# Kernel tuning notes

Measured on AMD Instinct MI355X. Metric: run time of the kernel, lower is better.

Reference implementation:

```python
import jax, jax.numpy as jnp
import numpy as np

N, E = 50000, 800000
IN, MAP, H, O = 256, 64, 4, 64
LEAKY_SLOPE = 0.2


def setup_inputs() -> dict:
    key = jax.random.key(0)
    ks = jax.random.split(key, 12)
    x = jax.random.normal(ks[0], (N, IN), dtype=jnp.float32)
    src = jax.random.randint(ks[1], (E,), 0, N, dtype=jnp.int32)
    dst = jax.random.randint(ks[2], (E,), 0, N, dtype=jnp.int32)
    s = 1.0 / np.sqrt(IN)
    W_gat = jax.random.normal(ks[3], (IN, H * O), dtype=jnp.float32) * s
    attn_l = jax.random.normal(ks[4], (H, O), dtype=jnp.float32) * 0.1
    attn_r = jax.random.normal(ks[5], (H, O), dtype=jnp.float32) * 0.1
    gate_m_W = jax.random.normal(ks[6], (IN, MAP), dtype=jnp.float32) * s
    gate_m_b = jnp.zeros((MAP,), dtype=jnp.float32)
    gate_fn_W = jax.random.normal(ks[7], (2 * IN + MAP, H), dtype=jnp.float32) * (1.0 / np.sqrt(2 * IN + MAP))
    gate_fn_b = jnp.zeros((H,), dtype=jnp.float32)
    merge_W = jax.random.normal(ks[8], (IN + O, O), dtype=jnp.float32) * (1.0 / np.sqrt(IN + O))
    merge_b = jnp.zeros((O,), dtype=jnp.float32)
    return {"x": x, "src": src, "dst": dst, "W_gat": W_gat, "attn_l": attn_l,
            "attn_r": attn_r, "gate_m_W": gate_m_W, "gate_m_b": gate_m_b,
            "gate_fn_W": gate_fn_W, "gate_fn_b": gate_fn_b,
            "merge_W": merge_W, "merge_b": merge_b}


def _forward(x, src, dst, W_gat, attn_l, attn_r, gate_m_W, gate_m_b,
             gate_fn_W, gate_fn_b, merge_W, merge_b):
    n = x.shape[0]
    # --- gate branch: gspmm mean of x, gspmm max of linear_z over in-neighbors ---
    deg = jax.ops.segment_sum(jnp.ones_like(dst, dtype=x.dtype), dst, num_segments=n)
    mean_z = jax.ops.segment_sum(x[src], dst, num_segments=n) / jnp.maximum(deg, 1.0)[:, None]
    z = x @ gate_m_W + gate_m_b  # [N, MAP]
    max_z = jax.ops.segment_max(z[src], dst, num_segments=n)
    max_z = jnp.where(deg[:, None] > 0, max_z, 0.0)  # empty neighborhoods -> 0
    nft = jnp.concatenate([x, max_z, mean_z], axis=1)  # [N, 2*IN+MAP]
    gate = jax.nn.sigmoid(nft @ gate_fn_W + gate_fn_b)  # [N, H]
    # --- GATConv ---
    feat = (x @ W_gat).reshape(n, H, O)  # [N, H, O]
    el = jnp.einsum('nho,ho->nh', feat, attn_l)
    er = jnp.einsum('nho,ho->nh', feat, attn_r)
    e = jax.nn.leaky_relu(el[src] + er[dst], negative_slope=LEAKY_SLOPE)  # [E, H]
    m = jax.ops.segment_max(e, dst, num_segments=n)  # [N, H]
    m = jnp.where(jnp.isfinite(m), m, 0.0)
    ex = jnp.exp(e - m[dst])  # [E, H]
    s = jax.ops.segment_sum(ex, dst, num_segments=n)  # [N, H]
    alpha = ex / jnp.maximum(s[dst], 1e-16)  # [E, H]
    attn_out = jax.ops.segment_sum(feat[src] * alpha[:, :, None], dst, num_segments=n)  # [N, H, O]
    # --- gated merge ---
    gated = (gate[:, :, None] * attn_out).mean(axis=1)  # [N, O]
    merge = jnp.concatenate([x, gated], axis=1) @ merge_W + merge_b  # [N, O]
    return merge


def reference(x, src, dst, W_gat, attn_l, attn_r, gate_m_W, gate_m_b,
              gate_fn_W, gate_fn_b, merge_W, merge_b):
    return _forward(x, src, dst, W_gat, attn_l, attn_r, gate_m_W, gate_m_b,
                    gate_fn_W, gate_fn_b, merge_W, merge_b)
```

## Files before the change

### kernel.cpp

```cpp
#include <hip/hip_runtime.h>
#include <math.h>

#define NN 50000
#define NE 800000
#define LEAKY 0.2f
#define NT 26
#define CAP 96
#define NBT (8 * NT * 64)
#define NRB 3125

typedef short bf16x8 __attribute__((ext_vector_type(8)));
typedef float f32x4 __attribute__((ext_vector_type(4)));
typedef float f32x2 __attribute__((ext_vector_type(2)));

__device__ __forceinline__ unsigned short f2bf(float f) {
  unsigned u = __float_as_uint(f);
  u += 0x7fffu + ((u >> 16) & 1u);
  return (unsigned short)(u >> 16);
}
__device__ __forceinline__ float bf2f(unsigned short h) {
  return __uint_as_float((unsigned)h << 16);
}
__device__ __forceinline__ float leaky(float v) { return v > 0.0f ? v : LEAKY * v; }
__device__ __forceinline__ float rlf(float v, int l) {
  return __uint_as_float(__builtin_amdgcn_readlane(__float_as_uint(v), l));
}
__device__ __forceinline__ int rli(int v, int l) {
  return __builtin_amdgcn_readlane(v, l);
}

#if defined(__has_builtin)
#if __has_builtin(__builtin_amdgcn_cvt_pk_f32_fp8) && \
    __has_builtin(__builtin_amdgcn_cvt_pk_fp8_f32) && \
    __has_builtin(__builtin_amdgcn_cvt_f32_fp8)
#define FP8_HW 1
#endif
#endif

#ifdef FP8_HW
__device__ __forceinline__ unsigned char f2fp8(float v) {
  return (unsigned char)(__builtin_amdgcn_cvt_pk_fp8_f32(v, v, 0u, false) & 0xFF);
}
__device__ __forceinline__ f32x2 fp8x2_lo(unsigned int v) {
  return __builtin_amdgcn_cvt_pk_f32_fp8(v, false);
}
__device__ __forceinline__ f32x2 fp8x2_hi(unsigned int v) {
  return __builtin_amdgcn_cvt_pk_f32_fp8(v, true);
}
__device__ __forceinline__ float fp8one(unsigned int v) {
  return __builtin_amdgcn_cvt_f32_fp8(v, 0);
}
#else
__device__ __forceinline__ unsigned char f2fp8(float f) {
  unsigned u = __float_as_uint(f);
  unsigned s = (u >> 31) << 7;
  unsigned a = u & 0x7FFFFFFFu;
  if (a >= 0x43E00000u) return (unsigned char)(s | 0x7E);
  if (a < 0x3C800000u) {
    float m = __uint_as_float(a) * 512.0f;
    int q = (int)(m + 0.5f); if (q > 7) q = 7;
    return (unsigned char)(s | q);
  }
  a += 0x7FFFFu + ((a >> 20) & 1);
  unsigned e = ((a >> 23) & 0xFF) - 120;
  if (e > 15) return (unsigned char)(s | 0x7E);
  return (unsigned char)(s | (e << 3) | ((a >> 20) & 7));
}
__device__ __forceinline__ float fp8dec1(unsigned b) {
  unsigned s = (b & 0x80u) << 24;
  unsigned em = b & 0x7Fu;
  unsigned e4 = em >> 3, m3 = em & 7;
  float v = e4 ? __uint_as_float(((e4 + 120) << 23) | (m3 << 20))
               : (float)m3 * 0.001953125f;
  return __uint_as_float(__float_as_uint(v) ^ s);
}
__device__ __forceinline__ f32x2 fp8x2_lo(unsigned int v) {
  f32x2 r;
  r[0] = fp8dec1(v & 0xFF);
  r[1] = fp8dec1((v >> 8) & 0xFF);
  return r;
}
__device__ __forceinline__ f32x2 fp8x2_hi(unsigned int v) {
  f32x2 r;
  r[0] = fp8dec1((v >> 16) & 0xFF);
  r[1] = fp8dec1((v >> 24) & 0xFF);
  return r;
}
__device__ __forceinline__ float fp8one(unsigned int v) { return fp8dec1(v & 0xFF); }
#endif

__global__ void k_init(int* __restrict__ cursor, unsigned char* __restrict__ zq,
                       float* __restrict__ epay) {
  int i = blockIdx.x * 256 + threadIdx.x;
  if (i < NN) cursor[i] = 0;
  if (blockIdx.x == 0) {
    int t = threadIdx.x;
    if (t < 64) zq[(size_t)NN * 64 + t] = 0xFE;
    if (t < 8) epay[(size_t)NN * 8 + t] = 0.0f;
  }
}

__global__ void k_scatter(const int* __restrict__ src, const int* __restrict__ dst,
                          int* __restrict__ cursor, int* __restrict__ csr_src) {
  int e = blockIdx.x * 256 + threadIdx.x;
  if (e < NE) {
    int n = dst[e];
    int pos = atomicAdd(&cursor[n], 1);
    if (pos < CAP) csr_src[n * CAP + pos] = src[e];
  }
}

__global__ __launch_bounds__(256) void k_pack(const float* __restrict__ x,
                                              unsigned short* __restrict__ xf) {
  int gid = blockIdx.x * 256 + threadIdx.x;
  int rowblk = gid >> 9;
  int rem = gid & 511;
  int kq = rem >> 6, lane = rem & 63;
  int m = lane & 15, kg = lane >> 4;
  const float* p = x + (size_t)(rowblk * 16 + m) * 256 + kq * 32 + kg * 8;
  float4 fa = *(const float4*)p;
  float4 fb = *(const float4*)(p + 4);
  ushort4 o0, o1;
  o0.x = f2bf(fa.x); o0.y = f2bf(fa.y); o0.z = f2bf(fa.z); o0.w = f2bf(fa.w);
  o1.x = f2bf(fb.x); o1.y = f2bf(fb.y); o1.z = f2bf(fb.z); o1.w = f2bf(fb.w);
  ushort4* dst = (ushort4*)(xf + (size_t)gid * 8);
  dst[0] = o0; dst[1] = o1;
}

__device__ __forceinline__ float panel_w(int col, int k,
    const float* W_gat, const float* gate_m_W, const float* merge_W,
    const float* gate_fn_W) {
  if (col < 256)      return W_gat[k * 256 + (col & 3) * 64 + (col >> 2)];
  else if (col < 320) return gate_m_W[k * 64 + (col - 256)];
  else if (col < 384) return merge_W[k * 64 + (col - 320)];
  else if (col < 388) return gate_fn_W[k * 4 + (col - 384)];
  else if (col < 392) return gate_fn_W[(320 + k) * 4 + (col - 388)];
  return 0.0f;
}

__global__ void k_bt(const float* __restrict__ W_gat, const float* __restrict__ gate_m_W,
                     const float* __restrict__ merge_W, const float* __restrict__ gate_fn_W,
                     unsigned short* __restrict__ Btf, unsigned short* __restrict__ mWf) {
  int idx = blockIdx.x * 256 + threadIdx.x;
  if (idx < NBT) {
    int kq = idx / (NT * 64);
    int rem = idx - kq * (NT * 64);
    int t = rem >> 6, lane = rem & 63;
    int col = t * 16 + (lane & 15);
    int k = kq * 32 + (lane >> 4) * 8;
    unsigned short* o = Btf + (size_t)idx * 8;
#pragma unroll
    for (int i = 0; i < 8; ++i)
      o[i] = f2bf(panel_w(col, k + i, W_gat, gate_m_W, merge_W, gate_fn_W));
  } else if (idx < NBT + 512) {
    int idx2 = idx - NBT;
    int kq = idx2 >> 8;
    int rem = idx2 & 255;
    int t = rem >> 6, lane = rem & 63;
    int col = t * 16 + (lane & 15);
    int k = kq * 32 + ((lane >> 4) & 3) * 8;
    unsigned short* o = mWf + (size_t)idx2 * 8;
#pragma unroll
    for (int i = 0; i < 8; ++i)
      o[i] = f2bf(merge_W[(size_t)(256 + k + i) * 64 + col]);
  }
}

__global__ __launch_bounds__(256) void k_gemm_mfma(
    const unsigned short* __restrict__ xf, const unsigned short* __restrict__ Btf,
    const float* __restrict__ gate_m_b,
    const float* __restrict__ attn_l, const float* __restrict__ attn_r,
    unsigned char* __restrict__ featq, unsigned char* __restrict__ zq,
    float* __restrict__ xm, float* __restrict__ gx, float* __restrict__ epay,
    float* __restrict__ erv) {
  __shared__ float els[32][4][2];
  __shared__ float ers[32][4][2];
  int lane = threadIdx.x & 63;
  int wave = threadIdx.x >> 6;
  int rowHalf = wave >> 1, colHalf = wave & 1;
  int rowB = blockIdx.x * 32;
  int row0 = rowB + rowHalf * 16;
  int t0 = colHalf * 13;
  int m = lane & 15;
  int kg = lane >> 4;
  f32x4 zero = {0.f, 0.f, 0.f, 0.f};
  f32x4 acc[13];
#pragma unroll
  for (int t = 0; t < 13; ++t) acc[t] = zero;

  const unsigned short* aB = xf + ((size_t)(blockIdx.x * 2 + rowHalf) * 8 * 64 + lane) * 8;
  const unsigned short* bB = Btf + (size_t)(t0 * 64 + lane) * 8;

  bf16x8 a0, a1, b0[13], b1[13];
  a0 = *(const bf16x8*)(aB);
#pragma unroll
  for (int t = 0; t < 13; ++t)
    b0[t] = *(const bf16x8*)(bB + (size_t)t * 64 * 8);
#pragma unroll 1
  for (int kq = 0; kq < 8; kq += 2) {
    a1 = *(const bf16x8*)(aB + (size_t)(kq + 1) * 64 * 8);
#pragma unroll
    for (int t = 0; t < 13; ++t)
      b1[t] = *(const bf16x8*)(bB + ((size_t)(kq + 1) * NT + t) * 64 * 8);
#pragma unroll
    for (int t = 0; t < 13; ++t)
      acc[t] = __builtin_amdgcn_mfma_f32_16x16x32_bf16(a0, b0[t], acc[t], 0, 0, 0);
    int kq2 = kq + 2 < 8 ? kq + 2 : 7;
    a0 = *(const bf16x8*)(aB + (size_t)kq2 * 64 * 8);
#pragma unroll
    for (int t = 0; t < 13; ++t)
      b0[t] = *(const bf16x8*)(bB + ((size_t)kq2 * NT + t) * 64 * 8);
#pragma unroll
    for (int t = 0; t < 13; ++t)
      acc[t] = __builtin_amdgcn_mfma_f32_16x16x32_bf16(a1, b1[t], acc[t], 0, 0, 0);
  }

  int h = m & 3, od = m >> 2;
  float elp[4] = {0, 0, 0, 0}, erp[4] = {0, 0, 0, 0};
#pragma unroll
  for (int t = 0; t < 13; ++t) {
    if ((t0 + t) * 16 < 256) {
      int o = (t0 + t) * 4 + od;
      float al = attn_l[h * 64 + o];
      float ar = attn_r[h * 64 + o];
#pragma unroll
      for (int r = 0; r < 4; ++r) {
        elp[r] += acc[t][r] * al;
        erp[r] += acc[t][r] * ar;
      }
    }
  }
#pragma unroll
  for (int r = 0; r < 4; ++r) {
    elp[r] += __shfl_xor(elp[r], 4, 64); elp[r] += __shfl_xor(elp[r], 8, 64);
    erp[r] += __shfl_xor(erp[r], 4, 64); erp[r] += __shfl_xor(erp[r], 8, 64);
  }
  if (m < 4) {
#pragma unroll
    for (int r = 0; r < 4; ++r) {
      els[rowHalf * 16 + kg * 4 + r][m][colHalf] = elp[r];
      ers[rowHalf * 16 + kg * 4 + r][m][colHalf] = erp[r];
    }
  }

  if (colHalf == 0) {
#pragma unroll
    for (int r = 0; r < 4; ++r) {
      int row = row0 + kg * 4 + r;
      if (row >= NN) continue;
#pragma unroll
      for (int t = 0; t < 13; ++t)
        featq[(size_t)row * 256 + t * 16 + m] = f2fp8(acc[t][r]);
    }
  } else {
#pragma unroll
    for (int r = 0; r < 4; ++r) {
      int row = row0 + kg * 4 + r;
      if (row >= NN) continue;
#pragma unroll
      for (int t = 0; t < 3; ++t)
        featq[(size_t)row * 256 + 208 + t * 16 + m] = f2fp8(acc[t][r]);
#pragma unroll
      for (int t = 3; t < 7; ++t) {
        int cc = (t - 3) * 16 + m;
        zq[(size_t)row * 64 + cc] = f2fp8(acc[t][r] + gate_m_b[cc]);
      }
#pragma unroll
      for (int t = 7; t < 11; ++t)
        xm[(size_t)row * 64 + (t - 7) * 16 + m] = acc[t][r];
      if (m < 4) gx[(size_t)row * 4 + m] = acc[11][r];
      else if (m < 8) epay[(size_t)row * 8 + m] = acc[11][r];
    }
  }
  __syncthreads();
  int tid = threadIdx.x;
  if (tid < 128) {
    int rr = tid >> 2, h2 = tid & 3;
    int row = rowB + rr;
    if (row < NN) {
      epay[(size_t)row * 8 + h2] = els[rr][h2][0] + els[rr][h2][1];
      erv[(size_t)row * 4 + h2] = ers[rr][h2][0] + ers[rr][h2][1];
    }
  }
}

__global__ __launch_bounds__(256) void k_node(
    const unsigned char* __restrict__ zq, const unsigned char* __restrict__ featq,
    const float* __restrict__ epay, const float* __restrict__ er,
    const float* __restrict__ gx,
    const int* __restrict__ cursor, const int* __restrict__ csr_src,
    const float* __restrict__ gate_fn_W, const float* __restrict__ gate_fn_b,
    unsigned short* __restrict__ gatedb) {
  __shared__ float WzT[4][64];
  int tid = threadIdx.x;
  {
    int c = tid >> 2, h = tid & 3;
    WzT[h][c] = gate_fn_W[(256 + c) * 4 + h];
  }
  __syncthreads();

  int lane = tid & 63;
  int node = blockIdx.x * 4 + (tid >> 6);
  if (node >= NN) return;
  int deg = cursor[node]; if (deg > CAP) deg = CAP;
  if (deg == 0) {
    gatedb[(size_t)node * 64 + lane] = 0;
    return;
  }
  int rs = node * CAP, re = rs + deg;
  int hh = lane >> 4, le = lane & 15;
  float er_h = er[(size_t)node * 4 + hh];

  float a0 = 0, a1 = 0, a2 = 0, a3 = 0;
  float psum = 0, usum = 0;
  float mz = -INFINITY;
  for (int j0 = rs; j0 < re; j0 += 16) {
    int jj = j0 + le;
    bool valid = jj < re;
    int s_l = valid ? csr_src[jj] : NN;
    float el_v = epay[((size_t)(unsigned)s_l << 3) + hh];
    float u_v  = epay[((size_t)(unsigned)s_l << 3) + 4 + hh];
    float lg = leaky(el_v + er_h);
    float p = valid ? __expf(lg) : 0.0f;
    psum += p;
    usum += valid ? u_v : 0.0f;
#pragma unroll
    for (int e2 = 0; e2 < 16; ++e2) {
      int s = rli(s_l, e2);
      float p0 = rlf(p, e2);
      float p1 = rlf(p, e2 + 16);
      float p2 = rlf(p, e2 + 32);
      float p3 = rlf(p, e2 + 48);
      unsigned int fv = *(const unsigned int*)(featq + ((size_t)(unsigned)s << 8) + lane * 4);
      unsigned int zv = zq[((size_t)(unsigned)s << 6) + lane];
      f32x2 lo = fp8x2_lo(fv);
      f32x2 hi = fp8x2_hi(fv);
      a0 += p0 * lo[0];
      a1 += p1 * lo[1];
      a2 += p2 * hi[0];
      a3 += p3 * hi[1];
      mz = fmaxf(mz, fp8one(zv));
    }
  }
#pragma unroll
  for (int off = 1; off < 16; off <<= 1) {
    psum += __shfl_xor(psum, off, 64);
    usum += __shfl_xor(usum, off, 64);
  }
  float s0 = rlf(psum, 0),  s1 = rlf(psum, 16);
  float s2 = rlf(psum, 32), s3 = rlf(psum, 48);
  float su0 = rlf(usum, 0),  su1 = rlf(usum, 16);
  float su2 = rlf(usum, 32), su3 = rlf(usum, 48);

  float g[4];
#pragma unroll
  for (int h = 0; h < 4; ++h) {
    float t = mz * WzT[h][lane];
#pragma unroll
    for (int off = 32; off; off >>= 1) t += __shfl_xor(t, off, 64);
    g[h] = t;
  }
  float inv_deg = 1.0f / (float)deg;
  float4 gx4 = *(const float4*)(gx + (size_t)node * 4);
  float g0 = 1.0f / (1.0f + __expf(-(g[0] + gx4.x + su0 * inv_deg + gate_fn_b[0])));
  float g1 = 1.0f / (1.0f + __expf(-(g[1] + gx4.y + su1 * inv_deg + gate_fn_b[1])));
  float g2 = 1.0f / (1.0f + __expf(-(g[2] + gx4.z + su2 * inv_deg + gate_fn_b[2])));
  float g3 = 1.0f / (1.0f + __expf(-(g[3] + gx4.w + su3 * inv_deg + gate_fn_b[3])));

  float gated = 0.25f * (g0 * a0 / s0 + g1 * a1 / s1 + g2 * a2 / s2 + g3 * a3 / s3);
  gatedb[(size_t)node * 64 + lane] = f2bf(gated);
}

__global__ __launch_bounds__(256) void k_merge(
    const unsigned short* __restrict__ gatedb, const unsigned short* __restrict__ mWf,
    const float* __restrict__ xm, const float* __restrict__ merge_b,
    float* __restrict__ out) {
  int lane = threadIdx.x & 63;
  int wave = threadIdx.x >> 6;
  int row0 = blockIdx.x * 64 + wave * 16;
  int m = lane & 15;
  int kg = lane >> 4;
  f32x4 zero = {0.f, 0.f, 0.f, 0.f};
  f32x4 acc[4] = {zero, zero, zero, zero};
  int arow = row0 + m; if (arow >= NN) arow = NN - 1;
  const unsigned short* ap = gatedb + (size_t)arow * 64 + kg * 8;
#pragma unroll
  for (int kq = 0; kq < 2; ++kq) {
    bf16x8 a = *(const bf16x8*)(ap + kq * 32);
#pragma unroll
    for (int t = 0; t < 4; ++t) {
      bf16x8 b = *(const bf16x8*)(mWf + (((size_t)kq * 4 + t) * 64 + lane) * 8);
      acc[t] = __builtin_amdgcn_mfma_f32_16x16x32_bf16(a, b, acc[t], 0, 0, 0);
    }
  }
#pragma unroll
  for (int r = 0; r < 4; ++r) {
    int row = row0 + kg * 4 + r;
    if (row >= NN) continue;
#pragma unroll
    for (int t = 0; t < 4; ++t) {
      int c = t * 16 + m;
      out[(size_t)row * 64 + c] = acc[t][r] + xm[(size_t)row * 64 + c] + merge_b[c];
    }
  }
}

extern "C" void kernel_launch(void* const* d_in, const int* in_sizes, int n_in,
                              void* d_out, int out_size, void* d_ws, size_t ws_size,
                              hipStream_t stream) {
  const float* x         = (const float*)d_in[0];
  const int*   src       = (const int*)d_in[1];
  const int*   dst       = (const int*)d_in[2];
  const float* W_gat     = (const float*)d_in[3];
  const float* attn_l    = (const float*)d_in[4];
  const float* attn_r    = (const float*)d_in[5];
  const float* gate_m_W  = (const float*)d_in[6];
  const float* gate_m_b  = (const float*)d_in[7];
  const float* gate_fn_W = (const float*)d_in[8];
  const float* gate_fn_b = (const float*)d_in[9];
  const float* merge_W   = (const float*)d_in[10];
  const float* merge_b   = (const float*)d_in[11];
  float* out = (float*)d_out;

  char* ws = (char*)d_ws;
  size_t off = 0;
  auto alloc = [&](size_t bytes) -> void* {
    off = (off + 255) & ~(size_t)255;
    void* p = ws + off;
    off += bytes;
    return p;
  };
  int* cursor    = (int*)alloc((size_t)NN * 4);
  int* csr_src   = (int*)alloc((size_t)NN * CAP * 4);
  float* epay = (float*)alloc((size_t)(NN + 1) * 8 * 4);
  float* er   = (float*)alloc((size_t)NN * 4 * 4);
  float* gx   = (float*)alloc((size_t)NN * 4 * 4);
  float* xm   = (float*)alloc((size_t)NN * 64 * 4);
  unsigned char* zq    = (unsigned char*)alloc((size_t)(NN + 1) * 64);
  unsigned char* featq = (unsigned char*)alloc((size_t)(NN + 1) * 256);
  unsigned short* gatedb = (unsigned short*)alloc((size_t)NN * 64 * 2);
  unsigned short* xf     = (unsigned short*)alloc((size_t)(NRB + 1) * 512 * 8 * 2);
  unsigned short* Btf    = (unsigned short*)alloc((size_t)NBT * 8 * 2);
  unsigned short* mWf    = (unsigned short*)alloc((size_t)512 * 8 * 2);

  k_init<<<(NN + 255) / 256, 256, 0, stream>>>(cursor, zq, epay);
  k_scatter<<<(NE + 255) / 256, 256, 0, stream>>>(src, dst, cursor, csr_src);
  k_pack<<<(NRB * 512) / 256, 256, 0, stream>>>(x, xf);
  k_bt<<<(NBT + 512 + 255) / 256, 256, 0, stream>>>(W_gat, gate_m_W, merge_W, gate_fn_W,
                                                    Btf, mWf);
  k_gemm_mfma<<<(NN + 31) / 32, 256, 0, stream>>>(xf, Btf, gate_m_b, attn_l, attn_r,
                                                  featq, zq, xm, gx, epay, er);
  k_node<<<(NN + 3) / 4, 256, 0, stream>>>(zq, featq, epay, er, gx, cursor, csr_src,
                                           gate_fn_W, gate_fn_b, gatedb);
  k_merge<<<(NN + 63) / 64, 256, 0, stream>>>(gatedb, mWf, xm, merge_b, out);
}
```

Measured before the change: 268.4 us.

## Fuse prep kernels, shrink CSR indices, interleave epay, use half2 aggregation

Result: no change. 265.8 us (-1.0%).

```diff
diff --git a/kernel.cpp b/kernel.cpp
--- a/kernel.cpp
+++ b/kernel.cpp
@@ -1,4 +1,5 @@
 #include <hip/hip_runtime.h>
+#include <hip/hip_fp16.h>
 #include <math.h>
 
 #define NN 50000
@@ -8,6 +9,9 @@
 #define CAP 96
 #define NBT (8 * NT * 64)
 #define NRB 3125
+#define PACK_BLKS 6250
+#define BT_BLKS 54
+#define INIT_BLKS 196
 
 typedef short bf16x8 __attribute__((ext_vector_type(8)));
 typedef float f32x4 __attribute__((ext_vector_type(4)));
@@ -18,9 +22,6 @@
   u += 0x7fffu + ((u >> 16) & 1u);
   return (unsigned short)(u >> 16);
 }
-__device__ __forceinline__ float bf2f(unsigned short h) {
-  return __uint_as_float((unsigned)h << 16);
-}
 __device__ __forceinline__ float leaky(float v) { return v > 0.0f ? v : LEAKY * v; }
 __device__ __forceinline__ float rlf(float v, int l) {
   return __uint_as_float(__builtin_amdgcn_readlane(__float_as_uint(v), l));
@@ -28,6 +29,8 @@
 __device__ __forceinline__ int rli(int v, int l) {
   return __builtin_amdgcn_readlane(v, l);
 }
+__device__ __forceinline__ int h2i(__half2 h) { union { __half2 h; int i; } u; u.h = h; return u.i; }
+__device__ __forceinline__ __half2 i2h(int i) { union { __half2 h; int i; } u; u.i = i; return u.h; }
 
 #if defined(__has_builtin)
 #if __has_builtin(__builtin_amdgcn_cvt_pk_f32_fp8) && \
@@ -75,57 +78,13 @@
   return __uint_as_float(__float_as_uint(v) ^ s);
 }
 __device__ __forceinline__ f32x2 fp8x2_lo(unsigned int v) {
-  f32x2 r;
-  r[0] = fp8dec1(v & 0xFF);
-  r[1] = fp8dec1((v >> 8) & 0xFF);
-  return r;
+  f32x2 r; r[0] = fp8dec1(v & 0xFF); r[1] = fp8dec1((v >> 8) & 0xFF); return r;
 }
 __device__ __forceinline__ f32x2 fp8x2_hi(unsigned int v) {
-  f32x2 r;
-  r[0] = fp8dec1((v >> 16) & 0xFF);
-  r[1] = fp8dec1((v >> 24) & 0xFF);
-  return r;
+  f32x2 r; r[0] = fp8dec1((v >> 16) & 0xFF); r[1] = fp8dec1((v >> 24) & 0xFF); return r;
 }
 __device__ __forceinline__ float fp8one(unsigned int v) { return fp8dec1(v & 0xFF); }
 #endif
-
-__global__ void k_init(int* __restrict__ cursor, unsigned char* __restrict__ zq,
-                       float* __restrict__ epay) {
-  int i = blockIdx.x * 256 + threadIdx.x;
-  if (i < NN) cursor[i] = 0;
-  if (blockIdx.x == 0) {
-    int t = threadIdx.x;
-    if (t < 64) zq[(size_t)NN * 64 + t] = 0xFE;
-    if (t < 8) epay[(size_t)NN * 8 + t] = 0.0f;
-  }
-}
-
-__global__ void k_scatter(const int* __restrict__ src, const int* __restrict__ dst,
-                          int* __restrict__ cursor, int* __restrict__ csr_src) {
-  int e = blockIdx.x * 256 + threadIdx.x;
-  if (e < NE) {
-    int n = dst[e];
-    int pos = atomicAdd(&cursor[n], 1);
-    if (pos < CAP) csr_src[n * CAP + pos] = src[e];
-  }
-}
-
-__global__ __launch_bounds__(256) void k_pack(const float* __restrict__ x,
-                                              unsigned short* __restrict__ xf) {
-  int gid = blockIdx.x * 256 + threadIdx.x;
-  int rowblk = gid >> 9;
-  int rem = gid & 511;
-  int kq = rem >> 6, lane = rem & 63;
-  int m = lane & 15, kg = lane >> 4;
-  const float* p = x + (size_t)(rowblk * 16 + m) * 256 + kq * 32 + kg * 8;
-  float4 fa = *(const float4*)p;
-  float4 fb = *(const float4*)(p + 4);
-  ushort4 o0, o1;
-  o0.x = f2bf(fa.x); o0.y = f2bf(fa.y); o0.z = f2bf(fa.z); o0.w = f2bf(fa.w);
-  o1.x = f2bf(fb.x); o1.y = f2bf(fb.y); o1.z = f2bf(fb.z); o1.w = f2bf(fb.w);
-  ushort4* dst = (ushort4*)(xf + (size_t)gid * 8);
-  dst[0] = o0; dst[1] = o1;
-}
 
 __device__ __forceinline__ float panel_w(int col, int k,
     const float* W_gat, const float* gate_m_W, const float* merge_W,
@@ -138,31 +97,70 @@
   return 0.0f;
 }
 
-__global__ void k_bt(const float* __restrict__ W_gat, const float* __restrict__ gate_m_W,
-                     const float* __restrict__ merge_W, const float* __restrict__ gate_fn_W,
-                     unsigned short* __restrict__ Btf, unsigned short* __restrict__ mWf) {
-  int idx = blockIdx.x * 256 + threadIdx.x;
-  if (idx < NBT) {
-    int kq = idx / (NT * 64);
-    int rem = idx - kq * (NT * 64);
-    int t = rem >> 6, lane = rem & 63;
-    int col = t * 16 + (lane & 15);
-    int k = kq * 32 + (lane >> 4) * 8;
-    unsigned short* o = Btf + (size_t)idx * 8;
-#pragma unroll
-    for (int i = 0; i < 8; ++i)
-      o[i] = f2bf(panel_w(col, k + i, W_gat, gate_m_W, merge_W, gate_fn_W));
-  } else if (idx < NBT + 512) {
-    int idx2 = idx - NBT;
-    int kq = idx2 >> 8;
-    int rem = idx2 & 255;
-    int t = rem >> 6, lane = rem & 63;
-    int col = t * 16 + (lane & 15);
-    int k = kq * 32 + ((lane >> 4) & 3) * 8;
-    unsigned short* o = mWf + (size_t)idx2 * 8;
-#pragma unroll
-    for (int i = 0; i < 8; ++i)
-      o[i] = f2bf(merge_W[(size_t)(256 + k + i) * 64 + col]);
+__global__ __launch_bounds__(256) void k_prep(
+    const float* __restrict__ x, const float* __restrict__ W_gat,
+    const float* __restrict__ gate_m_W, const float* __restrict__ merge_W,
+    const float* __restrict__ gate_fn_W,
+    unsigned short* __restrict__ xf, unsigned short* __restrict__ Btf,
+    unsigned short* __restrict__ mWf,
+    int* __restrict__ cursor, unsigned char* __restrict__ zq,
+    float* __restrict__ epay) {
+  int b = blockIdx.x, tid = threadIdx.x;
+  if (b < PACK_BLKS) {
+    int gid = b * 256 + tid;
+    int rowblk = gid >> 9;
+    int rem = gid & 511;
+    int kq = rem >> 6, lane = rem & 63;
+    int m = lane & 15, kg = lane >> 4;
+    const float* p = x + (size_t)(rowblk * 16 + m) * 256 + kq * 32 + kg * 8;
+    float4 fa = *(const float4*)p;
+    float4 fb = *(const float4*)(p + 4);
+    ushort4 o0, o1;
+    o0.x = f2bf(fa.x); o0.y = f2bf(fa.y); o0.z = f2bf(fa.z); o0.w = f2bf(fa.w);
+    o1.x = f2bf(fb.x); o1.y = f2bf(fb.y); o1.z = f2bf(fb.z); o1.w = f2bf(fb.w);
+    ushort4* dst = (ushort4*)(xf + (size_t)gid * 8);
+    dst[0] = o0; dst[1] = o1;
+  } else if (b < PACK_BLKS + BT_BLKS) {
+    int idx = (b - PACK_BLKS) * 256 + tid;
+    if (idx < NBT) {
+      int kq = idx / (NT * 64);
+      int rem = idx - kq * (NT * 64);
+      int t = rem >> 6, lane = rem & 63;
+      int col = t * 16 + (lane & 15);
+      int k = kq * 32 + (lane >> 4) * 8;
+      unsigned short* o = Btf + (size_t)idx * 8;
+#pragma unroll
+      for (int i = 0; i < 8; ++i)
+        o[i] = f2bf(panel_w(col, k + i, W_gat, gate_m_W, merge_W, gate_fn_W));
+    } else if (idx < NBT + 512) {
+      int idx2 = idx - NBT;
+      int kq = idx2 >> 8;
+      int rem = idx2 & 255;
+      int t = rem >> 6, lane = rem & 63;
+      int col = t * 16 + (lane & 15);
+      int k = kq * 32 + ((lane >> 4) & 3) * 8;
+      unsigned short* o = mWf + (size_t)idx2 * 8;
+#pragma unroll
+      for (int i = 0; i < 8; ++i)
+        o[i] = f2bf(merge_W[(size_t)(256 + k + i) * 64 + col]);
+    }
+  } else {
+    int i = (b - PACK_BLKS - BT_BLKS) * 256 + tid;
+    if (i < NN) cursor[i] = 0;
+    if (b == PACK_BLKS + BT_BLKS) {
+      if (tid < 64) zq[(size_t)NN * 64 + tid] = 0xFE;
+      if (tid < 8) epay[(size_t)NN * 8 + tid] = 0.0f;
+    }
+  }
+}
+
+__global__ void k_scatter(const int* __restrict__ src, const int* __restrict__ dst,
+                          int* __restrict__ cursor, unsigned short* __restrict__ csr_src) {
+  int e = blockIdx.x * 256 + threadIdx.x;
+  if (e < NE) {
+    int n = dst[e];
+    int pos = atomicAdd(&cursor[n], 1);
+    if (pos < CAP) csr_src[n * CAP + pos] = (unsigned short)src[e];
   }
 }
 
@@ -269,7 +267,7 @@
       for (int t = 7; t < 11; ++t)
         xm[(size_t)row * 64 + (t - 7) * 16 + m] = acc[t][r];
       if (m < 4) gx[(size_t)row * 4 + m] = acc[11][r];
-      else if (m < 8) epay[(size_t)row * 8 + m] = acc[11][r];
+      else if (m < 8) epay[(size_t)row * 8 + (m - 4) * 2 + 1] = acc[11][r];
     }
   }
   __syncthreads();
@@ -278,7 +276,7 @@
     int rr = tid >> 2, h2 = tid & 3;
     int row = rowB + rr;
     if (row < NN) {
-      epay[(size_t)row * 8 + h2] = els[rr][h2][0] + els[rr][h2][1];
+      epay[(size_t)row * 8 + h2 * 2] = els[rr][h2][0] + els[rr][h2][1];
       erv[(size_t)row * 4 + h2] = ers[rr][h2][0] + ers[rr][h2][1];
     }
   }
@@ -288,7 +286,7 @@
     const unsigned char* __restrict__ zq, const unsigned char* __restrict__ featq,
     const float* __restrict__ epay, const float* __restrict__ er,
     const float* __restrict__ gx,
-    const int* __restrict__ cursor, const int* __restrict__ csr_src,
+    const int* __restrict__ cursor, const unsigned short* __restrict__ csr_src,
     const float* __restrict__ gate_fn_W, const float* __restrict__ gate_fn_b,
     unsigned short* __restrict__ gatedb) {
   __shared__ float WzT[4][64];
@@ -311,37 +309,43 @@
   int hh = lane >> 4, le = lane & 15;
   float er_h = er[(size_t)node * 4 + hh];
 
-  float a0 = 0, a1 = 0, a2 = 0, a3 = 0;
+  __half2 a01 = __floats2half2_rn(0.f, 0.f);
+  __half2 a23 = __floats2half2_rn(0.f, 0.f);
   float psum = 0, usum = 0;
   float mz = -INFINITY;
   for (int j0 = rs; j0 < re; j0 += 16) {
     int jj = j0 + le;
     bool valid = jj < re;
-    int s_l = valid ? csr_src[jj] : NN;
-    float el_v = epay[((size_t)(unsigned)s_l << 3) + hh];
-    float u_v  = epay[((size_t)(unsigned)s_l << 3) + 4 + hh];
-    float lg = leaky(el_v + er_h);
+    int s_l = valid ? (int)csr_src[jj] : NN;
+    float2 eu = *(const float2*)(epay + ((size_t)(unsigned)s_l << 3) + hh * 2);
+    float lg = leaky(eu.x + er_h);
     float p = valid ? __expf(lg) : 0.0f;
     psum += p;
-    usum += valid ? u_v : 0.0f;
+    usum += valid ? eu.y : 0.0f;
+    float p0v = __shfl(p, le, 64);
+    float p1v = __shfl(p, le + 16, 64);
+    float p2v = __shfl(p, le + 32, 64);
+    float p3v = __shfl(p, le + 48, 64);
+    int pk01i = h2i(__floats2half2_rn(p0v, p1v));
+    int pk23i = h2i(__floats2half2_rn(p2v, p3v));
 #pragma unroll
     for (int e2 = 0; e2 < 16; ++e2) {
       int s = rli(s_l, e2);
-      float p0 = rlf(p, e2);
-      float p1 = rlf(p, e2 + 16);
-      float p2 = rlf(p, e2 + 32);
-      float p3 = rlf(p, e2 + 48);
+      __half2 b01 = i2h(rli(pk01i, e2));
+      __half2 b23 = i2h(rli(pk23i, e2));
       unsigned int fv = *(const unsigned int*)(featq + ((size_t)(unsigned)s << 8) + lane * 4);
       unsigned int zv = zq[((size_t)(unsigned)s << 6) + lane];
       f32x2 lo = fp8x2_lo(fv);
       f32x2 hi = fp8x2_hi(fv);
-      a0 += p0 * lo[0];
-      a1 += p1 * lo[1];
-      a2 += p2 * hi[0];
-      a3 += p3 * hi[1];
+      __half2 h01 = __floats2half2_rn(lo[0], lo[1]);
+      __half2 h23 = __floats2half2_rn(hi[0], hi[1]);
+      a01 = __hfma2(b01, h01, a01);
+      a23 = __hfma2(b23, h23, a23);
       mz = fmaxf(mz, fp8one(zv));
     }
   }
+  float a0 = __low2float(a01), a1 = __high2float(a01);
+  float a2 = __low2float(a23), a3 = __high2float(a23);
 #pragma unroll
   for (int off = 1; off < 16; off <<= 1) {
     psum += __shfl_xor(psum, off, 64);
@@ -431,7 +435,7 @@
     return p;
   };
   int* cursor    = (int*)alloc((size_t)NN * 4);
-  int* csr_src   = (int*)alloc((size_t)NN * CAP * 4);
+  unsigned short* csr_src = (unsigned short*)alloc((size_t)NN * CAP * 2);
   float* epay = (float*)alloc((size_t)(NN + 1) * 8 * 4);
   float* er   = (float*)alloc((size_t)NN * 4 * 4);
   float* gx   = (float*)alloc((size_t)NN * 4 * 4);
@@ -443,11 +447,9 @@
   unsigned short* Btf    = (unsigned short*)alloc((size_t)NBT * 8 * 2);
   unsigned short* mWf    = (unsigned short*)alloc((size_t)512 * 8 * 2);
 
-  k_init<<<(NN + 255) / 256, 256, 0, stream>>>(cursor, zq, epay);
+  k_prep<<<PACK_BLKS + BT_BLKS + INIT_BLKS, 256, 0, stream>>>(
+      x, W_gat, gate_m_W, merge_W, gate_fn_W, xf, Btf, mWf, cursor, zq, epay);
   k_scatter<<<(NE + 255) / 256, 256, 0, stream>>>(src, dst, cursor, csr_src);
-  k_pack<<<(NRB * 512) / 256, 256, 0, stream>>>(x, xf);
-  k_bt<<<(NBT + 512 + 255) / 256, 256, 0, stream>>>(W_gat, gate_m_W, merge_W, gate_fn_W,
-                                                    Btf, mWf);
   k_gemm_mfma<<<(NN + 31) / 32, 256, 0, stream>>>(xf, Btf, gate_m_b, attn_l, attn_r,
                                                   featq, zq, xm, gx, epay, er);
   k_node<<<(NN + 3) / 4, 256, 0, stream>>>(zq, featq, epay, er, gx, cursor, csr_src,
```
